# Performance work log

Measured on AMD Instinct MI355X. Metric: run time of the kernel, lower is better.

The kernel has to match this reference:

```python
import jax, jax.numpy as jnp
import numpy as np
from functools import partial

B, T, F, H = 32768, 48, 16, 32  # batch, horizon, feature dim, rnn_size


def setup_inputs() -> dict:
    key = jax.random.key(0)
    ks = jax.random.split(key, 9)
    return {
        "decoder_feature": jax.random.normal(ks[0], (B, T, F), dtype=jnp.float32),
        "decoder_init_input": jax.random.normal(ks[1], (B, 1), dtype=jnp.float32),
        "init_state": jax.random.normal(ks[2], (B, H), dtype=jnp.float32),
        # GRUCell (Keras default reset_after=True): kernel [in_dim, 3H], recurrent [H, 3H], two biases
        "kernel": jax.random.normal(ks[3], (1 + F, 3 * H), dtype=jnp.float32) * 0.1,
        "recurrent_kernel": jax.random.normal(ks[4], (H, 3 * H), dtype=jnp.float32) * 0.1,
        "bias_x": jax.random.normal(ks[5], (3 * H,), dtype=jnp.float32) * 0.1,
        "bias_h": jax.random.normal(ks[6], (3 * H,), dtype=jnp.float32) * 0.1,
        "dense_w": jax.random.normal(ks[7], (H, 1), dtype=jnp.float32) * 0.1,
        "dense_b": jax.random.normal(ks[8], (1,), dtype=jnp.float32) * 0.1,
    }


def reference(decoder_feature, decoder_init_input, init_state,
              kernel, recurrent_kernel, bias_x, bias_h, dense_w, dense_b):
    units = init_state.shape[-1]

    def step(carry, feat_t):
        h, prev_out = carry                              # h: [B,H], prev_out: [B,1]
        x = jnp.concatenate([prev_out, feat_t], axis=1)  # [B, 1+F]
        mx = x @ kernel + bias_x                         # [B, 3H]
        mh = h @ recurrent_kernel + bias_h               # [B, 3H] (reset_after=True)
        xz, xr, xh = jnp.split(mx, 3, axis=1)
        hz, hr, hh_in = jnp.split(mh, 3, axis=1)
        z = jax.nn.sigmoid(xz + hz)
        r = jax.nn.sigmoid(xr + hr)
        hh = jnp.tanh(xh + r * hh_in)
        h_new = z * h + (1.0 - z) * hh                   # GRU output == new state
        out = h_new @ dense_w + dense_b                  # Dense(1): [B,1]
        return (h_new, out), out

    feats = jnp.transpose(decoder_feature, (1, 0, 2))    # [T,B,F] time-major for scan
    _, outs = jax.lax.scan(step, (init_state, decoder_init_input), feats)
    return jnp.transpose(outs, (1, 0, 2))                # [B,T,1]
```

## Files before the change

kernel.cpp:

```cpp
#include <hip/hip_runtime.h>


typedef __attribute__((ext_vector_type(8))) short short8;
typedef __attribute__((ext_vector_type(4))) float f32x4;

constexpr int T_STEPS  = 48;
constexpr int F_DIM    = 16;
constexpr int H_DIM    = 32;
constexpr int ROW_SH   = 40;
constexpr int HX_SH    = 16 * ROW_SH;
constexpr int O_STRIDE = 17;

union S8 { short8 s; unsigned u[4]; };

__device__ __forceinline__ unsigned pk_bf16(float hi, float lo) {
    return __builtin_amdgcn_perm(__float_as_uint(hi) + 0x8000u,
                                 __float_as_uint(lo) + 0x8000u, 0x07060302u);
}
__device__ __forceinline__ short bf16s(float x) {
    return (short)((__float_as_uint(x) + 0x8000u) >> 16);
}
__device__ __forceinline__ float rcpf(float x) { return __builtin_amdgcn_rcpf(x); }
__device__ __forceinline__ float ex2(float x)  { return __builtin_amdgcn_exp2f(x); }
#define MFMA(a, b, c) __builtin_amdgcn_mfma_f32_16x16x32_bf16(a, b, c, 0, 0, 0)
#define SWZ16(v) __int_as_float(__builtin_amdgcn_ds_swizzle(__float_as_int(v), 0x401F))
#define BPERM(a, v) __builtin_amdgcn_ds_bpermute((a), (v))

__global__ __launch_bounds__(128, 4)
void gru_mfma8(const float* __restrict__ feat,
               const float* __restrict__ init_in,
               const float* __restrict__ init_h,
               const float* __restrict__ Wk,
               const float* __restrict__ Rk,
               const float* __restrict__ bx,
               const float* __restrict__ bh,
               const float* __restrict__ dw,
               const float* __restrict__ db,
               float* __restrict__ out)
{
    __shared__ __align__(16) short hx[2 * HX_SH];
    __shared__ float posum[2][2][16];
    __shared__ __align__(16) float obuf[T_STEPS * O_STRIDE];

    const int lane = threadIdx.x & 63;
    const int w    = threadIdx.x >> 6;
    const int ln   = lane & 15;
    const int quad = lane >> 4;
    const int b0   = blockIdx.x * 16;
    const int bpa  = (lane ^ 32) << 2;

    const float SZ = -1.44269504088896340736f;
    const float SC =  2.88539008177792681472f;

    S8 Wfz, Wfr, Wfh, Rfz, Rfr, Rfh;
#pragma unroll
    for (int j = 0; j < 8; ++j) {
        const int k = quad * 8 + j;
        const int n = w * 16 + ln;
        const float wz = (k < 16) ? SZ * Wk[(size_t)(k + 1) * 96 + n]      : 0.0f;
        const float wr = (k < 16) ? SZ * Wk[(size_t)(k + 1) * 96 + 32 + n] : 0.0f;
        const float wh = (k < 16) ? SC * Wk[(size_t)(k + 1) * 96 + 64 + n] : 0.0f;
        Wfz.s[j] = bf16s(wz); Wfr.s[j] = bf16s(wr); Wfh.s[j] = bf16s(wh);
        Rfz.s[j] = bf16s(SZ * Rk[(size_t)k * 96 + n]);
        Rfr.s[j] = bf16s(SZ * Rk[(size_t)k * 96 + 32 + n]);
        Rfh.s[j] = bf16s(SC * Rk[(size_t)k * 96 + 64 + n]);
    }

    float bz4[4], br4[4], bxh4[4], bhh4[4], wz4[4], wr4[4], wh4[4], dw4[4];
#pragma unroll
    for (int i = 0; i < 4; ++i) {
        const int c = w * 16 + quad * 4 + i;
        bz4[i]  = SZ * (bx[c] + bh[c]);
        br4[i]  = SZ * (bx[32 + c] + bh[32 + c]);
        bxh4[i] = SC * bx[64 + c];
        bhh4[i] = SC * bh[64 + c];
        wz4[i]  = SZ * Wk[c];
        wr4[i]  = SZ * Wk[32 + c];
        wh4[i]  = SC * Wk[64 + c];
        dw4[i]  = dw[c];
    }
    const float dbs = db[0];

    float hc[4];
#pragma unroll
    for (int i = 0; i < 4; ++i)
        hc[i] = init_h[(size_t)(b0 + ln) * H_DIM + w * 16 + quad * 4 + i];
    S8 hB;
    {
        const float* hp = init_h + (size_t)(b0 + ln) * H_DIM + quad * 8;
        const f32x4 a = *(const f32x4*)hp;
        const f32x4 b = *(const f32x4*)(hp + 4);
        hB.u[0] = pk_bf16(a[1], a[0]); hB.u[1] = pk_bf16(a[3], a[2]);
        hB.u[2] = pk_bf16(b[1], b[0]); hB.u[3] = pk_bf16(b[3], b[2]);
    }
    float po = init_in[b0 + ln];

    const float* fqb = feat + (size_t)(b0 + ln) * (T_STEPS * F_DIM) + (quad & 1) * 8;
    f32x4 pa0 = *(const f32x4*)(fqb);
    f32x4 pb0 = *(const f32x4*)(fqb + 4);
    f32x4 pa1 = *(const f32x4*)(fqb + F_DIM);
    f32x4 pb1 = *(const f32x4*)(fqb + F_DIM + 4);

    unsigned* hwr = (unsigned*)(hx + ln * ROW_SH + w * 16 + quad * 4);
    const short8* hrd = (const short8*)(hx + ln * ROW_SH + quad * 8);

#define GRU_STEP(T_, P_, PA_, PB_) do {                                        \
        S8 xa;                                                                 \
        xa.u[0] = pk_bf16(PA_[1], PA_[0]); xa.u[1] = pk_bf16(PA_[3], PA_[2]);  \
        xa.u[2] = pk_bf16(PB_[1], PB_[0]); xa.u[3] = pk_bf16(PB_[3], PB_[2]);  \
        const unsigned zm = (quad < 2) ? 0xFFFFFFFFu : 0u;                     \
        xa.u[0] &= zm; xa.u[1] &= zm; xa.u[2] &= zm; xa.u[3] &= zm;            \
            \
        const int t2 = ((T_) + 2 < T_STEPS) ? (T_) + 2 : T_STEPS - 1;          \
        PA_ = *(const f32x4*)(fqb + t2 * F_DIM);                               \
        PB_ = *(const f32x4*)(fqb + t2 * F_DIM + 4);                           \
                                      \
        f32x4 aZ  = {bz4[0],  bz4[1],  bz4[2],  bz4[3]};                       \
        f32x4 aR  = {br4[0],  br4[1],  br4[2],  br4[3]};                       \
        f32x4 aXH = {bxh4[0], bxh4[1], bxh4[2], bxh4[3]};                      \
        f32x4 aHH = {bhh4[0], bhh4[1], bhh4[2], bhh4[3]};                      \
        aZ  = MFMA(Wfz.s, xa.s, aZ);                                           \
        aR  = MFMA(Wfr.s, xa.s, aR);                                           \
        aXH = MFMA(Wfh.s, xa.s, aXH);                                          \
        aZ  = MFMA(Rfz.s, hB.s, aZ);                                           \
        aR  = MFMA(Rfr.s, hB.s, aR);                                           \
        aHH = MFMA(Rfh.s, hB.s, aHH);                                          \
                          \
        float hn[4];                                                           \
        _Pragma("unroll")                                                      \
        for (int i = 0; i < 4; ++i) {                                          \
            const float zz = rcpf(1.0f + ex2(fmaf(po, wz4[i], aZ[i])));        \
            const float rr = rcpf(1.0f + ex2(fmaf(po, wr4[i], aR[i])));        \
            const float vv = fmaf(rr, aHH[i], fmaf(po, wh4[i], aXH[i]));       \
            const float cc = fmaf(-2.0f, rcpf(1.0f + ex2(vv)), 1.0f);          \
            const float h2 = cc + zz * (hc[i] - cc);                           \
            hc[i] = h2;                                                        \
            hn[i] = h2;                                                        \
        }                                                                      \
                          \
        const float d01 = fmaf(hn[0], dw4[0], hn[1] * dw4[1]);                 \
        const float d23 = fmaf(hn[2], dw4[2], hn[3] * dw4[3]);                 \
        float s = d01 + d23;                                                   \
        s += SWZ16(s);                                                         \
        s += __int_as_float(BPERM(bpa, __float_as_int(s)));                    \
                       \
        unsigned* hw = hwr + (P_) * (HX_SH / 2);                               \
        hw[0] = pk_bf16(hn[1], hn[0]);                                         \
        hw[1] = pk_bf16(hn[3], hn[2]);                                         \
        if (lane < 16) posum[P_][w][lane] = s;                                 \
            \
        __builtin_amdgcn_s_waitcnt(0xC07F);                                    \
        __builtin_amdgcn_s_barrier();                                          \
                                      \
        hB.s = hrd[(P_) * (HX_SH / 8)];                                        \
        const float os = posum[P_][1 - w][ln];                                 \
        po = s + os + dbs;                                                     \
        if (w == 0 && lane < 16) obuf[(T_) * O_STRIDE + lane] = po;            \
    } while (0)

    for (int t = 0; t < T_STEPS; t += 2) {
        GRU_STEP(t,     0, pa0, pb0);
        GRU_STEP(t + 1, 1, pa1, pb1);
    }
#undef GRU_STEP

    if (w == 0) {
        const int row = lane >> 2;
        const int tb  = (lane & 3) * 12;
        float* orow = out + (size_t)(b0 + row) * T_STEPS + tb;
#pragma unroll
        for (int k = 0; k < 3; ++k) {
            f32x4 v;
#pragma unroll
            for (int e = 0; e < 4; ++e) v[e] = obuf[(tb + k * 4 + e) * O_STRIDE + row];
            *(f32x4*)(orow + k * 4) = v;
        }
    }
}

extern "C" void kernel_launch(void* const* d_in, const int* in_sizes, int n_in,
                              void* d_out, int out_size, void* d_ws, size_t ws_size,
                              hipStream_t stream) {
    const float* feat    = (const float*)d_in[0];
    const float* init_in = (const float*)d_in[1];
    const float* init_h  = (const float*)d_in[2];
    const float* Wk      = (const float*)d_in[3];
    const float* Rk      = (const float*)d_in[4];
    const float* bx      = (const float*)d_in[5];
    const float* bh      = (const float*)d_in[6];
    const float* dw      = (const float*)d_in[7];
    const float* db      = (const float*)d_in[8];
    float* out           = (float*)d_out;

    const int B = in_sizes[2] / H_DIM;
    dim3 grid((unsigned)(B / 16));
    dim3 block(128);
    hipLaunchKernelGGL(gru_mfma8, grid, block, 0, stream,
                       feat, init_in, init_h, Wk, Rk, bx, bh, dw, db, out);
}
```

Measured before the change: 192.3 us.

## Split GRU step across four waves with LDS gate exchange and two barriers

Each block now runs 256 threads: two waves do the input-projection MFMAs and two do the recurrent-projection MFMAs. Their gate pre-activations go to swizzled LDS planes, and all threads then do an elementwise update of two hidden units each, using a fused single-reciprocal form of the GRU update. This spreads the transcendental work over more lanes and shortens the per-step serial MFMA chain. In exchange it adds a second barrier per step plus extra LDS traffic, which may lengthen the serial recurrence latency.

```diff
diff --git a/kernel.cpp b/kernel.cpp
--- a/kernel.cpp
+++ b/kernel.cpp
@@ -3,13 +3,14 @@
 
 typedef __attribute__((ext_vector_type(8))) short short8;
 typedef __attribute__((ext_vector_type(4))) float f32x4;
-
-constexpr int T_STEPS  = 48;
-constexpr int F_DIM    = 16;
-constexpr int H_DIM    = 32;
-constexpr int ROW_SH   = 40;
-constexpr int HX_SH    = 16 * ROW_SH;
-constexpr int O_STRIDE = 17;
+typedef __attribute__((ext_vector_type(2))) float f32x2;
+
+constexpr int T_STEPS   = 48;
+constexpr int F_DIM     = 16;
+constexpr int H_DIM     = 32;
+constexpr int O_STRIDE  = 17;
+constexpr int HP_STRIDE = 20;
+constexpr int PLANE_DW  = 512;
 
 union S8 { short8 s; unsigned u[4]; };
 
@@ -23,11 +24,10 @@
 __device__ __forceinline__ float rcpf(float x) { return __builtin_amdgcn_rcpf(x); }
 __device__ __forceinline__ float ex2(float x)  { return __builtin_amdgcn_exp2f(x); }
 #define MFMA(a, b, c) __builtin_amdgcn_mfma_f32_16x16x32_bf16(a, b, c, 0, 0, 0)
-#define SWZ16(v) __int_as_float(__builtin_amdgcn_ds_swizzle(__float_as_int(v), 0x401F))
-#define BPERM(a, v) __builtin_amdgcn_ds_bpermute((a), (v))
-
-__global__ __launch_bounds__(128, 4)
-void gru_mfma8(const float* __restrict__ feat,
+#define SWZ(v, off) __int_as_float(__builtin_amdgcn_ds_swizzle(__float_as_int(v), (off)))
+
+__global__ __launch_bounds__(256, 8)
+void gru_mfma9(const float* __restrict__ feat,
                const float* __restrict__ init_in,
                const float* __restrict__ init_h,
                const float* __restrict__ Wk,
@@ -38,135 +38,145 @@
                const float* __restrict__ db,
                float* __restrict__ out)
 {
-    __shared__ __align__(16) short hx[2 * HX_SH];
-    __shared__ float posum[2][2][16];
-    __shared__ __align__(16) float obuf[T_STEPS * O_STRIDE];
-
-    const int lane = threadIdx.x & 63;
-    const int w    = threadIdx.x >> 6;
+    __shared__ __align__(16) float    gp[6 * PLANE_DW];
+    __shared__ __align__(16) unsigned hpl[16 * HP_STRIDE];
+    __shared__ float posum[16];
+    __shared__ __align__(16) float    obuf[T_STEPS * O_STRIDE];
+
+    const int tid  = threadIdx.x;
+    const int lane = tid & 63;
+    const int wv   = tid >> 6;
+    const int half = wv & 1;
+    const int kh   = wv >> 1;
     const int ln   = lane & 15;
     const int quad = lane >> 4;
     const int b0   = blockIdx.x * 16;
-    const int bpa  = (lane ^ 32) << 2;
+    const int ab   = tid >> 4;
+    const int ah   = (tid & 15) * 2;
 
     const float SZ = -1.44269504088896340736f;
     const float SC =  2.88539008177792681472f;
 
-    S8 Wfz, Wfr, Wfh, Rfz, Rfr, Rfh;
+    S8 Az, Ar, Ah;
 #pragma unroll
     for (int j = 0; j < 8; ++j) {
         const int k = quad * 8 + j;
-        const int n = w * 16 + ln;
-        const float wz = (k < 16) ? SZ * Wk[(size_t)(k + 1) * 96 + n]      : 0.0f;
-        const float wr = (k < 16) ? SZ * Wk[(size_t)(k + 1) * 96 + 32 + n] : 0.0f;
-        const float wh = (k < 16) ? SC * Wk[(size_t)(k + 1) * 96 + 64 + n] : 0.0f;
-        Wfz.s[j] = bf16s(wz); Wfr.s[j] = bf16s(wr); Wfh.s[j] = bf16s(wh);
-        Rfz.s[j] = bf16s(SZ * Rk[(size_t)k * 96 + n]);
-        Rfr.s[j] = bf16s(SZ * Rk[(size_t)k * 96 + 32 + n]);
-        Rfh.s[j] = bf16s(SC * Rk[(size_t)k * 96 + 64 + n]);
-    }
-
-    float bz4[4], br4[4], bxh4[4], bhh4[4], wz4[4], wr4[4], wh4[4], dw4[4];
+        const int n = half * 16 + ln;
+        if (kh) {
+            Az.s[j] = bf16s(SZ * Rk[(size_t)k * 96 + n]);
+            Ar.s[j] = bf16s(SZ * Rk[(size_t)k * 96 + 32 + n]);
+            Ah.s[j] = bf16s(SC * Rk[(size_t)k * 96 + 64 + n]);
+        } else {
+            const float wz = (k < 16) ? Wk[(size_t)(k + 1) * 96 + n]      : 0.0f;
+            const float wr = (k < 16) ? Wk[(size_t)(k + 1) * 96 + 32 + n] : 0.0f;
+            const float wh = (k < 16) ? Wk[(size_t)(k + 1) * 96 + 64 + n] : 0.0f;
+            Az.s[j] = bf16s(SZ * wz); Ar.s[j] = bf16s(SZ * wr); Ah.s[j] = bf16s(SC * wh);
+        }
+    }
+
+    f32x4 cz, cr, ch;
 #pragma unroll
     for (int i = 0; i < 4; ++i) {
-        const int c = w * 16 + quad * 4 + i;
-        bz4[i]  = SZ * (bx[c] + bh[c]);
-        br4[i]  = SZ * (bx[32 + c] + bh[32 + c]);
-        bxh4[i] = SC * bx[64 + c];
-        bhh4[i] = SC * bh[64 + c];
-        wz4[i]  = SZ * Wk[c];
-        wr4[i]  = SZ * Wk[32 + c];
-        wh4[i]  = SC * Wk[64 + c];
-        dw4[i]  = dw[c];
-    }
+        const int c = half * 16 + quad * 4 + i;
+        cz[i] = kh ? 0.0f : SZ * (bx[c] + bh[c]);
+        cr[i] = kh ? 0.0f : SZ * (bx[32 + c] + bh[32 + c]);
+        ch[i] = SC * (kh ? bh[64 + c] : bx[64 + c]);
+    }
+
+    float hc0 = init_h[(size_t)(b0 + ab) * H_DIM + ah];
+    float hc1 = init_h[(size_t)(b0 + ab) * H_DIM + ah + 1];
+    const float dw0 = dw[ah], dw1 = dw[ah + 1];
+    const float wzp0 = SZ * Wk[ah],      wzp1 = SZ * Wk[ah + 1];
+    const float wrp0 = SZ * Wk[32 + ah], wrp1 = SZ * Wk[32 + ah + 1];
+    const float whp0 = SC * Wk[64 + ah], whp1 = SC * Wk[64 + ah + 1];
     const float dbs = db[0];
 
-    float hc[4];
-#pragma unroll
-    for (int i = 0; i < 4; ++i)
-        hc[i] = init_h[(size_t)(b0 + ln) * H_DIM + w * 16 + quad * 4 + i];
-    S8 hB;
-    {
-        const float* hp = init_h + (size_t)(b0 + ln) * H_DIM + quad * 8;
-        const f32x4 a = *(const f32x4*)hp;
-        const f32x4 b = *(const f32x4*)(hp + 4);
-        hB.u[0] = pk_bf16(a[1], a[0]); hB.u[1] = pk_bf16(a[3], a[2]);
-        hB.u[2] = pk_bf16(b[1], b[0]); hB.u[3] = pk_bf16(b[3], b[2]);
-    }
-    float po = init_in[b0 + ln];
+    hpl[ab * HP_STRIDE + (ah >> 1)] = pk_bf16(hc1, hc0);
+    if ((tid & 15) == 0) posum[ab] = init_in[b0 + ab];
 
     const float* fqb = feat + (size_t)(b0 + ln) * (T_STEPS * F_DIM) + (quad & 1) * 8;
-    f32x4 pa0 = *(const f32x4*)(fqb);
-    f32x4 pb0 = *(const f32x4*)(fqb + 4);
-    f32x4 pa1 = *(const f32x4*)(fqb + F_DIM);
-    f32x4 pb1 = *(const f32x4*)(fqb + F_DIM + 4);
-
-    unsigned* hwr = (unsigned*)(hx + ln * ROW_SH + w * 16 + quad * 4);
-    const short8* hrd = (const short8*)(hx + ln * ROW_SH + quad * 8);
-
-#define GRU_STEP(T_, P_, PA_, PB_) do {                                        \
-        S8 xa;                                                                 \
-        xa.u[0] = pk_bf16(PA_[1], PA_[0]); xa.u[1] = pk_bf16(PA_[3], PA_[2]);  \
-        xa.u[2] = pk_bf16(PB_[1], PB_[0]); xa.u[3] = pk_bf16(PB_[3], PB_[2]);  \
-        const unsigned zm = (quad < 2) ? 0xFFFFFFFFu : 0u;                     \
-        xa.u[0] &= zm; xa.u[1] &= zm; xa.u[2] &= zm; xa.u[3] &= zm;            \
-            \
-        const int t2 = ((T_) + 2 < T_STEPS) ? (T_) + 2 : T_STEPS - 1;          \
-        PA_ = *(const f32x4*)(fqb + t2 * F_DIM);                               \
-        PB_ = *(const f32x4*)(fqb + t2 * F_DIM + 4);                           \
-                                      \
-        f32x4 aZ  = {bz4[0],  bz4[1],  bz4[2],  bz4[3]};                       \
-        f32x4 aR  = {br4[0],  br4[1],  br4[2],  br4[3]};                       \
-        f32x4 aXH = {bxh4[0], bxh4[1], bxh4[2], bxh4[3]};                      \
-        f32x4 aHH = {bhh4[0], bhh4[1], bhh4[2], bhh4[3]};                      \
-        aZ  = MFMA(Wfz.s, xa.s, aZ);                                           \
-        aR  = MFMA(Wfr.s, xa.s, aR);                                           \
-        aXH = MFMA(Wfh.s, xa.s, aXH);                                          \
-        aZ  = MFMA(Rfz.s, hB.s, aZ);                                           \
-        aR  = MFMA(Rfr.s, hB.s, aR);                                           \
-        aHH = MFMA(Rfh.s, hB.s, aHH);                                          \
-                          \
-        float hn[4];                                                           \
-        _Pragma("unroll")                                                      \
-        for (int i = 0; i < 4; ++i) {                                          \
-            const float zz = rcpf(1.0f + ex2(fmaf(po, wz4[i], aZ[i])));        \
-            const float rr = rcpf(1.0f + ex2(fmaf(po, wr4[i], aR[i])));        \
-            const float vv = fmaf(rr, aHH[i], fmaf(po, wh4[i], aXH[i]));       \
-            const float cc = fmaf(-2.0f, rcpf(1.0f + ex2(vv)), 1.0f);          \
-            const float h2 = cc + zz * (hc[i] - cc);                           \
-            hc[i] = h2;                                                        \
-            hn[i] = h2;                                                        \
-        }                                                                      \
-                          \
-        const float d01 = fmaf(hn[0], dw4[0], hn[1] * dw4[1]);                 \
-        const float d23 = fmaf(hn[2], dw4[2], hn[3] * dw4[3]);                 \
-        float s = d01 + d23;                                                   \
-        s += SWZ16(s);                                                         \
-        s += __int_as_float(BPERM(bpa, __float_as_int(s)));                    \
-                       \
-        unsigned* hw = hwr + (P_) * (HX_SH / 2);                               \
-        hw[0] = pk_bf16(hn[1], hn[0]);                                         \
-        hw[1] = pk_bf16(hn[3], hn[2]);                                         \
-        if (lane < 16) posum[P_][w][lane] = s;                                 \
-            \
-        __builtin_amdgcn_s_waitcnt(0xC07F);                                    \
-        __builtin_amdgcn_s_barrier();                                          \
-                                      \
-        hB.s = hrd[(P_) * (HX_SH / 8)];                                        \
-        const float os = posum[P_][1 - w][ln];                                 \
-        po = s + os + dbs;                                                     \
-        if (w == 0 && lane < 16) obuf[(T_) * O_STRIDE + lane] = po;            \
-    } while (0)
-
-    for (int t = 0; t < T_STEPS; t += 2) {
-        GRU_STEP(t,     0, pa0, pb0);
-        GRU_STEP(t + 1, 1, pa1, pb1);
-    }
-#undef GRU_STEP
-
-    if (w == 0) {
-        const int row = lane >> 2;
-        const int tb  = (lane & 3) * 12;
+    f32x4 pa, pb;
+    if (!kh) { pa = *(const f32x4*)fqb; pb = *(const f32x4*)(fqb + 4); }
+
+    const int gw  = kh * 3 * PLANE_DW + ln * 32
+                  + ((half * 16 + quad * 4) ^ ((ln & 7) << 2));
+    const int grd = ab * 32 + (ah ^ ((ab & 7) << 2));
+    const int hrd = ln * HP_STRIDE + quad * 4;
+    const int hwr = ab * HP_STRIDE + (ah >> 1);
+
+    __syncthreads();
+    S8 bop;
+    if (kh) bop.s = *(const short8*)&hpl[hrd];
+
+    for (int t = 0; t < T_STEPS; ++t) {
+        if (!kh) {
+            if (quad < 2) {
+                bop.u[0] = pk_bf16(pa[1], pa[0]); bop.u[1] = pk_bf16(pa[3], pa[2]);
+                bop.u[2] = pk_bf16(pb[1], pb[0]); bop.u[3] = pk_bf16(pb[3], pb[2]);
+            } else {
+                bop.u[0] = 0; bop.u[1] = 0; bop.u[2] = 0; bop.u[3] = 0;
+            }
+            const int t1 = (t < T_STEPS - 1) ? t + 1 : t;
+            pa = *(const f32x4*)(fqb + t1 * F_DIM);
+            pb = *(const f32x4*)(fqb + t1 * F_DIM + 4);
+        }
+        f32x4 aZ = cz, aR = cr, aH = ch;
+        aZ = MFMA(Az.s, bop.s, aZ);
+        aR = MFMA(Ar.s, bop.s, aR);
+        aH = MFMA(Ah.s, bop.s, aH);
+        *(f32x4*)&gp[gw]                = aZ;
+        *(f32x4*)&gp[gw + PLANE_DW]     = aR;
+        *(f32x4*)&gp[gw + 2 * PLANE_DW] = aH;
+        __builtin_amdgcn_s_waitcnt(0xC07F);
+        __builtin_amdgcn_s_barrier();
+
+        const float po1 = posum[ab];
+        const f32x2 xz = *(const f32x2*)&gp[grd];
+        const f32x2 xr = *(const f32x2*)&gp[grd + PLANE_DW];
+        const f32x2 xh = *(const f32x2*)&gp[grd + 2 * PLANE_DW];
+        const f32x2 hz = *(const f32x2*)&gp[grd + 3 * PLANE_DW];
+        const f32x2 hr = *(const f32x2*)&gp[grd + 4 * PLANE_DW];
+        const f32x2 hh = *(const f32x2*)&gp[grd + 5 * PLANE_DW];
+
+        float h0n, h1n;
+        {
+            const float Sr = fmaf(po1, wrp0, xr[0] + hr[0]);
+            const float rr = rcpf(1.0f + ex2(Sr));
+            const float vv = fmaf(rr, hh[0], fmaf(po1, whp0, xh[0]));
+            const float Ez = ex2(fmaf(po1, wzp0, xz[0] + hz[0]));
+            const float Dv = 1.0f + ex2(vv);
+            const float num = fmaf(hc0, Dv, (Dv - 2.0f) * Ez);
+            const float den = fmaf(Dv, Ez, Dv);
+            h0n = num * rcpf(den);
+        }
+        {
+            const float Sr = fmaf(po1, wrp1, xr[1] + hr[1]);
+            const float rr = rcpf(1.0f + ex2(Sr));
+            const float vv = fmaf(rr, hh[1], fmaf(po1, whp1, xh[1]));
+            const float Ez = ex2(fmaf(po1, wzp1, xz[1] + hz[1]));
+            const float Dv = 1.0f + ex2(vv);
+            const float num = fmaf(hc1, Dv, (Dv - 2.0f) * Ez);
+            const float den = fmaf(Dv, Ez, Dv);
+            h1n = num * rcpf(den);
+        }
+        hc0 = h0n; hc1 = h1n;
+        hpl[hwr] = pk_bf16(h1n, h0n);
+
+        float s = fmaf(h0n, dw0, h1n * dw1);
+        s += SWZ(s, 0x041F);
+        s += SWZ(s, 0x081F);
+        s += SWZ(s, 0x101F);
+        s += SWZ(s, 0x201F);
+        const float po = s + dbs;
+        if ((tid & 15) == 0) { posum[ab] = po; obuf[t * O_STRIDE + ab] = po; }
+        __builtin_amdgcn_s_waitcnt(0xC07F);
+        __builtin_amdgcn_s_barrier();
+        if (kh) bop.s = *(const short8*)&hpl[hrd];
+    }
+
+    if (tid < 64) {
+        const int row = tid >> 2;
+        const int tb  = (tid & 3) * 12;
         float* orow = out + (size_t)(b0 + row) * T_STEPS + tb;
 #pragma unroll
         for (int k = 0; k < 3; ++k) {
@@ -194,7 +204,7 @@
 
     const int B = in_sizes[2] / H_DIM;
     dim3 grid((unsigned)(B / 16));
-    dim3 block(128);
-    hipLaunchKernelGGL(gru_mfma8, grid, block, 0, stream,
+    dim3 block(256);
+    hipLaunchKernelGGL(gru_mfma9, grid, block, 0, stream,
                        feat, init_in, init_h, Wk, Rk, bx, bh, dw, db, out);
 }
```

Result: slower. 320.7 us (+66.7%).

## Process two batch tiles per block and fold prev-output into MFMA

Applied to the files above, without the earlier changes.

Each block now handles 32 batch rows as two independent 16-row chains, interleaving their MFMAs and activations so each barrier-bound recurrence step carries twice the work and exposes ILP. The previous-output input is folded into the x-side MFMA through the padded K slots, using a hi/lo bf16 split to keep precision. The GRU update is rewritten to use one fewer reciprocal by combining the sigmoid and tanh denominators. The cost is more registers and LDS per block, with launch bounds lowered to 2 blocks per SIMD and half as many blocks in the grid.

```diff
diff --git a/kernel.cpp b/kernel.cpp
--- a/kernel.cpp
+++ b/kernel.cpp
@@ -26,27 +26,27 @@
 #define SWZ16(v) __int_as_float(__builtin_amdgcn_ds_swizzle(__float_as_int(v), 0x401F))
 #define BPERM(a, v) __builtin_amdgcn_ds_bpermute((a), (v))
 
-__global__ __launch_bounds__(128, 4)
-void gru_mfma8(const float* __restrict__ feat,
-               const float* __restrict__ init_in,
-               const float* __restrict__ init_h,
-               const float* __restrict__ Wk,
-               const float* __restrict__ Rk,
-               const float* __restrict__ bx,
-               const float* __restrict__ bh,
-               const float* __restrict__ dw,
-               const float* __restrict__ db,
-               float* __restrict__ out)
+__global__ __launch_bounds__(128, 2)
+void gru_mfma10(const float* __restrict__ feat,
+                const float* __restrict__ init_in,
+                const float* __restrict__ init_h,
+                const float* __restrict__ Wk,
+                const float* __restrict__ Rk,
+                const float* __restrict__ bx,
+                const float* __restrict__ bh,
+                const float* __restrict__ dw,
+                const float* __restrict__ db,
+                float* __restrict__ out)
 {
-    __shared__ __align__(16) short hx[2 * HX_SH];
-    __shared__ float posum[2][2][16];
-    __shared__ __align__(16) float obuf[T_STEPS * O_STRIDE];
+    __shared__ __align__(16) short hx[4 * HX_SH];
+    __shared__ float posumf[2 * 2 * 2 * 16];
+    __shared__ __align__(16) float obuf[2 * T_STEPS * O_STRIDE];
 
     const int lane = threadIdx.x & 63;
     const int w    = threadIdx.x >> 6;
     const int ln   = lane & 15;
     const int quad = lane >> 4;
-    const int b0   = blockIdx.x * 16;
+    const int b0   = blockIdx.x * 32;
     const int bpa  = (lane ^ 32) << 2;
 
     const float SZ = -1.44269504088896340736f;
@@ -57,16 +57,23 @@
     for (int j = 0; j < 8; ++j) {
         const int k = quad * 8 + j;
         const int n = w * 16 + ln;
-        const float wz = (k < 16) ? SZ * Wk[(size_t)(k + 1) * 96 + n]      : 0.0f;
-        const float wr = (k < 16) ? SZ * Wk[(size_t)(k + 1) * 96 + 32 + n] : 0.0f;
-        const float wh = (k < 16) ? SC * Wk[(size_t)(k + 1) * 96 + 64 + n] : 0.0f;
-        Wfz.s[j] = bf16s(wz); Wfr.s[j] = bf16s(wr); Wfh.s[j] = bf16s(wh);
+        float wz = 0.0f, wr = 0.0f, wh = 0.0f;
+        if (k < 16) {
+            wz = Wk[(size_t)(k + 1) * 96 + n];
+            wr = Wk[(size_t)(k + 1) * 96 + 32 + n];
+            wh = Wk[(size_t)(k + 1) * 96 + 64 + n];
+        } else if (k < 18) {
+            wz = Wk[n];
+            wr = Wk[32 + n];
+            wh = Wk[64 + n];
+        }
+        Wfz.s[j] = bf16s(SZ * wz); Wfr.s[j] = bf16s(SZ * wr); Wfh.s[j] = bf16s(SC * wh);
         Rfz.s[j] = bf16s(SZ * Rk[(size_t)k * 96 + n]);
         Rfr.s[j] = bf16s(SZ * Rk[(size_t)k * 96 + 32 + n]);
         Rfh.s[j] = bf16s(SC * Rk[(size_t)k * 96 + 64 + n]);
     }
 
-    float bz4[4], br4[4], bxh4[4], bhh4[4], wz4[4], wr4[4], wh4[4], dw4[4];
+    float bz4[4], br4[4], bxh4[4], bhh4[4], dw4[4];
 #pragma unroll
     for (int i = 0; i < 4; ++i) {
         const int c = w * 16 + quad * 4 + i;
@@ -74,105 +81,161 @@
         br4[i]  = SZ * (bx[32 + c] + bh[32 + c]);
         bxh4[i] = SC * bx[64 + c];
         bhh4[i] = SC * bh[64 + c];
-        wz4[i]  = SZ * Wk[c];
-        wr4[i]  = SZ * Wk[32 + c];
-        wh4[i]  = SC * Wk[64 + c];
         dw4[i]  = dw[c];
     }
     const float dbs = db[0];
 
-    float hc[4];
-#pragma unroll
-    for (int i = 0; i < 4; ++i)
-        hc[i] = init_h[(size_t)(b0 + ln) * H_DIM + w * 16 + quad * 4 + i];
-    S8 hB;
+    float hc0[4], hc1[4];
+#pragma unroll
+    for (int i = 0; i < 4; ++i) {
+        hc0[i] = init_h[(size_t)(b0 + ln) * H_DIM + w * 16 + quad * 4 + i];
+        hc1[i] = init_h[(size_t)(b0 + 16 + ln) * H_DIM + w * 16 + quad * 4 + i];
+    }
+    S8 hB0, hB1;
     {
-        const float* hp = init_h + (size_t)(b0 + ln) * H_DIM + quad * 8;
-        const f32x4 a = *(const f32x4*)hp;
-        const f32x4 b = *(const f32x4*)(hp + 4);
-        hB.u[0] = pk_bf16(a[1], a[0]); hB.u[1] = pk_bf16(a[3], a[2]);
-        hB.u[2] = pk_bf16(b[1], b[0]); hB.u[3] = pk_bf16(b[3], b[2]);
-    }
-    float po = init_in[b0 + ln];
-
-    const float* fqb = feat + (size_t)(b0 + ln) * (T_STEPS * F_DIM) + (quad & 1) * 8;
-    f32x4 pa0 = *(const f32x4*)(fqb);
-    f32x4 pb0 = *(const f32x4*)(fqb + 4);
-    f32x4 pa1 = *(const f32x4*)(fqb + F_DIM);
-    f32x4 pb1 = *(const f32x4*)(fqb + F_DIM + 4);
+        const float* hp0 = init_h + (size_t)(b0 + ln) * H_DIM + quad * 8;
+        const float* hp1 = init_h + (size_t)(b0 + 16 + ln) * H_DIM + quad * 8;
+        f32x4 a = *(const f32x4*)hp0, b = *(const f32x4*)(hp0 + 4);
+        hB0.u[0] = pk_bf16(a[1], a[0]); hB0.u[1] = pk_bf16(a[3], a[2]);
+        hB0.u[2] = pk_bf16(b[1], b[0]); hB0.u[3] = pk_bf16(b[3], b[2]);
+        a = *(const f32x4*)hp1; b = *(const f32x4*)(hp1 + 4);
+        hB1.u[0] = pk_bf16(a[1], a[0]); hB1.u[1] = pk_bf16(a[3], a[2]);
+        hB1.u[2] = pk_bf16(b[1], b[0]); hB1.u[3] = pk_bf16(b[3], b[2]);
+    }
+    float po0 = init_in[b0 + ln];
+    float po1 = init_in[b0 + 16 + ln];
+
+    const float* fq0 = feat + (size_t)(b0 + ln) * (T_STEPS * F_DIM) + (quad & 1) * 8;
+    const float* fq1 = feat + (size_t)(b0 + 16 + ln) * (T_STEPS * F_DIM) + (quad & 1) * 8;
+    f32x4 p0a0 = *(const f32x4*)(fq0);
+    f32x4 p0b0 = *(const f32x4*)(fq0 + 4);
+    f32x4 p0a1 = *(const f32x4*)(fq0 + F_DIM);
+    f32x4 p0b1 = *(const f32x4*)(fq0 + F_DIM + 4);
+    f32x4 p1a0 = *(const f32x4*)(fq1);
+    f32x4 p1b0 = *(const f32x4*)(fq1 + 4);
+    f32x4 p1a1 = *(const f32x4*)(fq1 + F_DIM);
+    f32x4 p1b1 = *(const f32x4*)(fq1 + F_DIM + 4);
 
     unsigned* hwr = (unsigned*)(hx + ln * ROW_SH + w * 16 + quad * 4);
     const short8* hrd = (const short8*)(hx + ln * ROW_SH + quad * 8);
 
-#define GRU_STEP(T_, P_, PA_, PB_) do {                                        \
-        S8 xa;                                                                 \
-        xa.u[0] = pk_bf16(PA_[1], PA_[0]); xa.u[1] = pk_bf16(PA_[3], PA_[2]);  \
-        xa.u[2] = pk_bf16(PB_[1], PB_[0]); xa.u[3] = pk_bf16(PB_[3], PB_[2]);  \
-        const unsigned zm = (quad < 2) ? 0xFFFFFFFFu : 0u;                     \
-        xa.u[0] &= zm; xa.u[1] &= zm; xa.u[2] &= zm; xa.u[3] &= zm;            \
-            \
-        const int t2 = ((T_) + 2 < T_STEPS) ? (T_) + 2 : T_STEPS - 1;          \
-        PA_ = *(const f32x4*)(fqb + t2 * F_DIM);                               \
-        PB_ = *(const f32x4*)(fqb + t2 * F_DIM + 4);                           \
-                                      \
-        f32x4 aZ  = {bz4[0],  bz4[1],  bz4[2],  bz4[3]};                       \
-        f32x4 aR  = {br4[0],  br4[1],  br4[2],  br4[3]};                       \
-        f32x4 aXH = {bxh4[0], bxh4[1], bxh4[2], bxh4[3]};                      \
-        f32x4 aHH = {bhh4[0], bhh4[1], bhh4[2], bhh4[3]};                      \
-        aZ  = MFMA(Wfz.s, xa.s, aZ);                                           \
-        aR  = MFMA(Wfr.s, xa.s, aR);                                           \
-        aXH = MFMA(Wfh.s, xa.s, aXH);                                          \
-        aZ  = MFMA(Rfz.s, hB.s, aZ);                                           \
-        aR  = MFMA(Rfr.s, hB.s, aR);                                           \
-        aHH = MFMA(Rfh.s, hB.s, aHH);                                          \
-                          \
-        float hn[4];                                                           \
+#define STEP2(T_, P_, PA_, PB_, QA_, QB_) do {                                 \
+        S8 xa0, xa1;                                                           \
+        {                                                                      \
+            const unsigned zm = (quad < 2) ? 0xFFFFFFFFu : 0u;                 \
+            xa0.u[0] = pk_bf16(PA_[1], PA_[0]) & zm;                           \
+            xa0.u[1] = pk_bf16(PA_[3], PA_[2]) & zm;                           \
+            xa0.u[2] = pk_bf16(PB_[1], PB_[0]) & zm;                           \
+            xa0.u[3] = pk_bf16(PB_[3], PB_[2]) & zm;                           \
+            xa1.u[0] = pk_bf16(QA_[1], QA_[0]) & zm;                           \
+            xa1.u[1] = pk_bf16(QA_[3], QA_[2]) & zm;                           \
+            xa1.u[2] = pk_bf16(QB_[1], QB_[0]) & zm;                           \
+            xa1.u[3] = pk_bf16(QB_[3], QB_[2]) & zm;                           \
+            if (quad == 2) {            \
+                const float h0 = __uint_as_float(                              \
+                    (__float_as_uint(po0) + 0x8000u) & 0xFFFF0000u);           \
+                const float h1 = __uint_as_float(                              \
+                    (__float_as_uint(po1) + 0x8000u) & 0xFFFF0000u);           \
+                xa0.u[0] = pk_bf16(po0 - h0, h0);                              \
+                xa1.u[0] = pk_bf16(po1 - h1, h1);                              \
+            }                                                                  \
+        }                                                                      \
+        {         \
+            const int t2 = ((T_) + 2 < T_STEPS) ? (T_) + 2 : T_STEPS - 1;      \
+            PA_ = *(const f32x4*)(fq0 + t2 * F_DIM);                           \
+            PB_ = *(const f32x4*)(fq0 + t2 * F_DIM + 4);                       \
+            QA_ = *(const f32x4*)(fq1 + t2 * F_DIM);                           \
+            QB_ = *(const f32x4*)(fq1 + t2 * F_DIM + 4);                       \
+        }                                                                      \
+                                \
+        f32x4 aZ0 = {bz4[0], bz4[1], bz4[2], bz4[3]};                          \
+        f32x4 aR0 = {br4[0], br4[1], br4[2], br4[3]};                          \
+        f32x4 aH0 = {bxh4[0], bxh4[1], bxh4[2], bxh4[3]};                      \
+        f32x4 aG0 = {bhh4[0], bhh4[1], bhh4[2], bhh4[3]};                      \
+        f32x4 aZ1 = aZ0, aR1 = aR0, aH1 = aH0, aG1 = aG0;                      \
+        aZ0 = MFMA(Wfz.s, xa0.s, aZ0);  aZ1 = MFMA(Wfz.s, xa1.s, aZ1);         \
+        aR0 = MFMA(Wfr.s, xa0.s, aR0);  aR1 = MFMA(Wfr.s, xa1.s, aR1);         \
+        aH0 = MFMA(Wfh.s, xa0.s, aH0);  aH1 = MFMA(Wfh.s, xa1.s, aH1);         \
+        aZ0 = MFMA(Rfz.s, hB0.s, aZ0);  aZ1 = MFMA(Rfz.s, hB1.s, aZ1);         \
+        aR0 = MFMA(Rfr.s, hB0.s, aR0);  aR1 = MFMA(Rfr.s, hB1.s, aR1);         \
+        aG0 = MFMA(Rfh.s, hB0.s, aG0);  aG1 = MFMA(Rfh.s, hB1.s, aG1);         \
+                              \
+        float hn0[4], hn1[4];                                                  \
         _Pragma("unroll")                                                      \
         for (int i = 0; i < 4; ++i) {                                          \
-            const float zz = rcpf(1.0f + ex2(fmaf(po, wz4[i], aZ[i])));        \
-            const float rr = rcpf(1.0f + ex2(fmaf(po, wr4[i], aR[i])));        \
-            const float vv = fmaf(rr, aHH[i], fmaf(po, wh4[i], aXH[i]));       \
-            const float cc = fmaf(-2.0f, rcpf(1.0f + ex2(vv)), 1.0f);          \
-            const float h2 = cc + zz * (hc[i] - cc);                           \
-            hc[i] = h2;                                                        \
-            hn[i] = h2;                                                        \
-        }                                                                      \
-                          \
-        const float d01 = fmaf(hn[0], dw4[0], hn[1] * dw4[1]);                 \
-        const float d23 = fmaf(hn[2], dw4[2], hn[3] * dw4[3]);                 \
-        float s = d01 + d23;                                                   \
-        s += SWZ16(s);                                                         \
-        s += __int_as_float(BPERM(bpa, __float_as_int(s)));                    \
-                       \
-        unsigned* hw = hwr + (P_) * (HX_SH / 2);                               \
-        hw[0] = pk_bf16(hn[1], hn[0]);                                         \
-        hw[1] = pk_bf16(hn[3], hn[2]);                                         \
-        if (lane < 16) posum[P_][w][lane] = s;                                 \
-            \
+            {                                                                  \
+                const float Ez = ex2(aZ0[i]);                                  \
+                const float rr = rcpf(1.0f + ex2(aR0[i]));                     \
+                const float vv = fmaf(rr, aG0[i], aH0[i]);                     \
+                const float Dv = 1.0f + ex2(vv);                               \
+                const float num = fmaf(hc0[i], Dv, (Dv - 2.0f) * Ez);          \
+                const float den = fmaf(Dv, Ez, Dv);                            \
+                const float h2 = num * rcpf(den);                              \
+                hc0[i] = h2; hn0[i] = h2;                                      \
+            }                                                                  \
+            {                                                                  \
+                const float Ez = ex2(aZ1[i]);                                  \
+                const float rr = rcpf(1.0f + ex2(aR1[i]));                     \
+                const float vv = fmaf(rr, aG1[i], aH1[i]);                     \
+                const float Dv = 1.0f + ex2(vv);                               \
+                const float num = fmaf(hc1[i], Dv, (Dv - 2.0f) * Ez);          \
+                const float den = fmaf(Dv, Ez, Dv);                            \
+                const float h2 = num * rcpf(den);                              \
+                hc1[i] = h2; hn1[i] = h2;                                      \
+            }                                                                  \
+        }                                                                      \
+                                             \
+        float s0 = fmaf(hn0[0], dw4[0], hn0[1] * dw4[1])                       \
+                 + fmaf(hn0[2], dw4[2], hn0[3] * dw4[3]);                      \
+        float s1 = fmaf(hn1[0], dw4[0], hn1[1] * dw4[1])                       \
+                 + fmaf(hn1[2], dw4[2], hn1[3] * dw4[3]);                      \
+        s0 += SWZ16(s0); s1 += SWZ16(s1);                                      \
+        s0 += __int_as_float(BPERM(bpa, __float_as_int(s0)));                  \
+        s1 += __int_as_float(BPERM(bpa, __float_as_int(s1)));                  \
+                             \
+        {                                                                      \
+            unsigned* hw0 = hwr + (0 * 2 + (P_)) * (HX_SH / 2);                \
+            unsigned* hw1 = hwr + (2 + (P_)) * (HX_SH / 2);                    \
+            hw0[0] = pk_bf16(hn0[1], hn0[0]);                                  \
+            hw0[1] = pk_bf16(hn0[3], hn0[2]);                                  \
+            hw1[0] = pk_bf16(hn1[1], hn1[0]);                                  \
+            hw1[1] = pk_bf16(hn1[3], hn1[2]);                                  \
+            if (lane < 16) {                                                   \
+                posumf[((0 * 2 + (P_)) * 2 + w) * 16 + lane] = s0;             \
+                posumf[((2 + (P_)) * 2 + w) * 16 + lane] = s1;                 \
+            }                                                                  \
+        }                                                                      \
+                \
         __builtin_amdgcn_s_waitcnt(0xC07F);                                    \
         __builtin_amdgcn_s_barrier();                                          \
-                                      \
-        hB.s = hrd[(P_) * (HX_SH / 8)];                                        \
-        const float os = posum[P_][1 - w][ln];                                 \
-        po = s + os + dbs;                                                     \
-        if (w == 0 && lane < 16) obuf[(T_) * O_STRIDE + lane] = po;            \
+                                    \
+        hB0.s = hrd[(0 * 2 + (P_)) * (HX_SH / 8)];                             \
+        hB1.s = hrd[(2 + (P_)) * (HX_SH / 8)];                                 \
+        po0 = s0 + posumf[((0 * 2 + (P_)) * 2 + (1 - w)) * 16 + ln] + dbs;     \
+        po1 = s1 + posumf[((2 + (P_)) * 2 + (1 - w)) * 16 + ln] + dbs;         \
+        if (lane < 16) {                                                       \
+            if (w == 0) obuf[(T_) * O_STRIDE + lane] = po0;                    \
+            else        obuf[T_STEPS * O_STRIDE + (T_) * O_STRIDE + lane] = po1;\
+        }                                                                      \
     } while (0)
 
     for (int t = 0; t < T_STEPS; t += 2) {
-        GRU_STEP(t,     0, pa0, pb0);
-        GRU_STEP(t + 1, 1, pa1, pb1);
-    }
-#undef GRU_STEP
-
-    if (w == 0) {
+        STEP2(t,     0, p0a0, p0b0, p1a0, p1b0);
+        STEP2(t + 1, 1, p0a1, p0b1, p1a1, p1b1);
+    }
+#undef STEP2
+
+    __syncthreads();
+    {
+        const float* ob = obuf + w * (T_STEPS * O_STRIDE);
         const int row = lane >> 2;
         const int tb  = (lane & 3) * 12;
-        float* orow = out + (size_t)(b0 + row) * T_STEPS + tb;
+        float* orow = out + (size_t)(b0 + w * 16 + row) * T_STEPS + tb;
 #pragma unroll
         for (int k = 0; k < 3; ++k) {
             f32x4 v;
 #pragma unroll
-            for (int e = 0; e < 4; ++e) v[e] = obuf[(tb + k * 4 + e) * O_STRIDE + row];
+            for (int e = 0; e < 4; ++e) v[e] = ob[(tb + k * 4 + e) * O_STRIDE + row];
             *(f32x4*)(orow + k * 4) = v;
         }
     }
@@ -193,8 +256,8 @@
     float* out           = (float*)d_out;
 
     const int B = in_sizes[2] / H_DIM;
-    dim3 grid((unsigned)(B / 16));
+    dim3 grid((unsigned)(B / 32));
     dim3 block(128);
-    hipLaunchKernelGGL(gru_mfma8, grid, block, 0, stream,
+    hipLaunchKernelGGL(gru_mfma10, grid, block, 0, stream,
                        feat, init_in, init_h, Wk, Rk, bx, bh, dw, db, out);
 }
```

New measurement: 184.7 us. 1.04x faster.

## Run each 16-row GRU tile in one wavefront with register-resident hidden state

Applied to the files above, without the earlier changes.

Each 16-row batch tile now runs on a single 64-lane wavefront instead of two. A column permutation makes the MFMA output layout match the B-operand layout of the next step, so the hidden state is repacked in registers and the per-step LDS exchange and block barrier go away. The previous-output term is folded into the MFMA as a split-bf16 hi/lo input row, and the z-gate/tanh blend is rewritten to use one reciprocal instead of two. Each wave now issues twice the MFMAs and transcendentals per step, and the single-wave blocks may change occupancy and latency hiding.

```diff
diff --git a/kernel.cpp b/kernel.cpp
--- a/kernel.cpp
+++ b/kernel.cpp
@@ -7,8 +7,6 @@
 constexpr int T_STEPS  = 48;
 constexpr int F_DIM    = 16;
 constexpr int H_DIM    = 32;
-constexpr int ROW_SH   = 40;
-constexpr int HX_SH    = 16 * ROW_SH;
 constexpr int O_STRIDE = 17;
 
 union S8 { short8 s; unsigned u[4]; };
@@ -26,24 +24,21 @@
 #define SWZ16(v) __int_as_float(__builtin_amdgcn_ds_swizzle(__float_as_int(v), 0x401F))
 #define BPERM(a, v) __builtin_amdgcn_ds_bpermute((a), (v))
 
-__global__ __launch_bounds__(128, 4)
-void gru_mfma8(const float* __restrict__ feat,
-               const float* __restrict__ init_in,
-               const float* __restrict__ init_h,
-               const float* __restrict__ Wk,
-               const float* __restrict__ Rk,
-               const float* __restrict__ bx,
-               const float* __restrict__ bh,
-               const float* __restrict__ dw,
-               const float* __restrict__ db,
-               float* __restrict__ out)
+__global__ __launch_bounds__(64, 2)
+void gru_mfma11(const float* __restrict__ feat,
+                const float* __restrict__ init_in,
+                const float* __restrict__ init_h,
+                const float* __restrict__ Wk,
+                const float* __restrict__ Rk,
+                const float* __restrict__ bx,
+                const float* __restrict__ bh,
+                const float* __restrict__ dw,
+                const float* __restrict__ db,
+                float* __restrict__ out)
 {
-    __shared__ __align__(16) short hx[2 * HX_SH];
-    __shared__ float posum[2][2][16];
     __shared__ __align__(16) float obuf[T_STEPS * O_STRIDE];
 
-    const int lane = threadIdx.x & 63;
-    const int w    = threadIdx.x >> 6;
+    const int lane = threadIdx.x;
     const int ln   = lane & 15;
     const int quad = lane >> 4;
     const int b0   = blockIdx.x * 16;
@@ -52,47 +47,55 @@
     const float SZ = -1.44269504088896340736f;
     const float SC =  2.88539008177792681472f;
 
-    S8 Wfz, Wfr, Wfh, Rfz, Rfr, Rfh;
+    const int cA0 = (ln >> 2) * 8 + (ln & 3);
+    const int cA1 = cA0 + 4;
+
+    S8 WzA, WrA, WhA, WzB, WrB, WhB, RzA, RrA, RhA, RzB, RrB, RhB;
 #pragma unroll
     for (int j = 0; j < 8; ++j) {
         const int k = quad * 8 + j;
-        const int n = w * 16 + ln;
-        const float wz = (k < 16) ? SZ * Wk[(size_t)(k + 1) * 96 + n]      : 0.0f;
-        const float wr = (k < 16) ? SZ * Wk[(size_t)(k + 1) * 96 + 32 + n] : 0.0f;
-        const float wh = (k < 16) ? SC * Wk[(size_t)(k + 1) * 96 + 64 + n] : 0.0f;
-        Wfz.s[j] = bf16s(wz); Wfr.s[j] = bf16s(wr); Wfh.s[j] = bf16s(wh);
-        Rfz.s[j] = bf16s(SZ * Rk[(size_t)k * 96 + n]);
-        Rfr.s[j] = bf16s(SZ * Rk[(size_t)k * 96 + 32 + n]);
-        Rfh.s[j] = bf16s(SC * Rk[(size_t)k * 96 + 64 + n]);
-    }
-
-    float bz4[4], br4[4], bxh4[4], bhh4[4], wz4[4], wr4[4], wh4[4], dw4[4];
+        float wzA = 0, wrA = 0, whA = 0, wzB = 0, wrB = 0, whB = 0;
+        if (k < 16) {
+            const float* Wrow = Wk + (size_t)(k + 1) * 96;
+            wzA = Wrow[cA0]; wrA = Wrow[32 + cA0]; whA = Wrow[64 + cA0];
+            wzB = Wrow[cA1]; wrB = Wrow[32 + cA1]; whB = Wrow[64 + cA1];
+        } else if (k < 18) {
+            wzA = Wk[cA0]; wrA = Wk[32 + cA0]; whA = Wk[64 + cA0];
+            wzB = Wk[cA1]; wrB = Wk[32 + cA1]; whB = Wk[64 + cA1];
+        }
+        WzA.s[j] = bf16s(SZ * wzA); WrA.s[j] = bf16s(SZ * wrA); WhA.s[j] = bf16s(SC * whA);
+        WzB.s[j] = bf16s(SZ * wzB); WrB.s[j] = bf16s(SZ * wrB); WhB.s[j] = bf16s(SC * whB);
+        const float* Rrow = Rk + (size_t)k * 96;
+        RzA.s[j] = bf16s(SZ * Rrow[cA0]); RrA.s[j] = bf16s(SZ * Rrow[32 + cA0]);
+        RhA.s[j] = bf16s(SC * Rrow[64 + cA0]);
+        RzB.s[j] = bf16s(SZ * Rrow[cA1]); RrB.s[j] = bf16s(SZ * Rrow[32 + cA1]);
+        RhB.s[j] = bf16s(SC * Rrow[64 + cA1]);
+    }
+
+    f32x4 czA, crA, chA, cgA, czB, crB, chB, cgB, dwA, dwB;
 #pragma unroll
     for (int i = 0; i < 4; ++i) {
-        const int c = w * 16 + quad * 4 + i;
-        bz4[i]  = SZ * (bx[c] + bh[c]);
-        br4[i]  = SZ * (bx[32 + c] + bh[32 + c]);
-        bxh4[i] = SC * bx[64 + c];
-        bhh4[i] = SC * bh[64 + c];
-        wz4[i]  = SZ * Wk[c];
-        wr4[i]  = SZ * Wk[32 + c];
-        wh4[i]  = SC * Wk[64 + c];
-        dw4[i]  = dw[c];
+        const int c0 = quad * 8 + i, c1 = c0 + 4;
+        czA[i] = SZ * (bx[c0] + bh[c0]);           czB[i] = SZ * (bx[c1] + bh[c1]);
+        crA[i] = SZ * (bx[32 + c0] + bh[32 + c0]); crB[i] = SZ * (bx[32 + c1] + bh[32 + c1]);
+        chA[i] = SC * bx[64 + c0];                 chB[i] = SC * bx[64 + c1];
+        cgA[i] = SC * bh[64 + c0];                 cgB[i] = SC * bh[64 + c1];
+        dwA[i] = dw[c0];                           dwB[i] = dw[c1];
     }
     const float dbs = db[0];
 
-    float hc[4];
-#pragma unroll
-    for (int i = 0; i < 4; ++i)
-        hc[i] = init_h[(size_t)(b0 + ln) * H_DIM + w * 16 + quad * 4 + i];
+    f32x4 hcA, hcB;
+#pragma unroll
+    for (int i = 0; i < 4; ++i) {
+        hcA[i] = init_h[(size_t)(b0 + ln) * H_DIM + quad * 8 + i];
+        hcB[i] = init_h[(size_t)(b0 + ln) * H_DIM + quad * 8 + 4 + i];
+    }
     S8 hB;
-    {
-        const float* hp = init_h + (size_t)(b0 + ln) * H_DIM + quad * 8;
-        const f32x4 a = *(const f32x4*)hp;
-        const f32x4 b = *(const f32x4*)(hp + 4);
-        hB.u[0] = pk_bf16(a[1], a[0]); hB.u[1] = pk_bf16(a[3], a[2]);
-        hB.u[2] = pk_bf16(b[1], b[0]); hB.u[3] = pk_bf16(b[3], b[2]);
-    }
+    hB.u[0] = pk_bf16(hcA[1], hcA[0]);
+    hB.u[1] = pk_bf16(hcA[3], hcA[2]);
+    hB.u[2] = pk_bf16(hcB[1], hcB[0]);
+    hB.u[3] = pk_bf16(hcB[3], hcB[2]);
+
     float po = init_in[b0 + ln];
 
     const float* fqb = feat + (size_t)(b0 + ln) * (T_STEPS * F_DIM) + (quad & 1) * 8;
@@ -101,70 +104,83 @@
     f32x4 pa1 = *(const f32x4*)(fqb + F_DIM);
     f32x4 pb1 = *(const f32x4*)(fqb + F_DIM + 4);
 
-    unsigned* hwr = (unsigned*)(hx + ln * ROW_SH + w * 16 + quad * 4);
-    const short8* hrd = (const short8*)(hx + ln * ROW_SH + quad * 8);
-
-#define GRU_STEP(T_, P_, PA_, PB_) do {                                        \
+#define GRU_STEP(T_, PA_, PB_) do {                                            \
         S8 xa;                                                                 \
-        xa.u[0] = pk_bf16(PA_[1], PA_[0]); xa.u[1] = pk_bf16(PA_[3], PA_[2]);  \
-        xa.u[2] = pk_bf16(PB_[1], PB_[0]); xa.u[3] = pk_bf16(PB_[3], PB_[2]);  \
-        const unsigned zm = (quad < 2) ? 0xFFFFFFFFu : 0u;                     \
-        xa.u[0] &= zm; xa.u[1] &= zm; xa.u[2] &= zm; xa.u[3] &= zm;            \
-            \
-        const int t2 = ((T_) + 2 < T_STEPS) ? (T_) + 2 : T_STEPS - 1;          \
-        PA_ = *(const f32x4*)(fqb + t2 * F_DIM);                               \
-        PB_ = *(const f32x4*)(fqb + t2 * F_DIM + 4);                           \
-                                      \
-        f32x4 aZ  = {bz4[0],  bz4[1],  bz4[2],  bz4[3]};                       \
-        f32x4 aR  = {br4[0],  br4[1],  br4[2],  br4[3]};                       \
-        f32x4 aXH = {bxh4[0], bxh4[1], bxh4[2], bxh4[3]};                      \
-        f32x4 aHH = {bhh4[0], bhh4[1], bhh4[2], bhh4[3]};                      \
-        aZ  = MFMA(Wfz.s, xa.s, aZ);                                           \
-        aR  = MFMA(Wfr.s, xa.s, aR);                                           \
-        aXH = MFMA(Wfh.s, xa.s, aXH);                                          \
-        aZ  = MFMA(Rfz.s, hB.s, aZ);                                           \
-        aR  = MFMA(Rfr.s, hB.s, aR);                                           \
-        aHH = MFMA(Rfh.s, hB.s, aHH);                                          \
-                          \
-        float hn[4];                                                           \
+        {                                                                      \
+            const unsigned zm = (quad < 2) ? 0xFFFFFFFFu : 0u;                 \
+            xa.u[0] = pk_bf16(PA_[1], PA_[0]) & zm;                            \
+            xa.u[1] = pk_bf16(PA_[3], PA_[2]) & zm;                            \
+            xa.u[2] = pk_bf16(PB_[1], PB_[0]) & zm;                            \
+            xa.u[3] = pk_bf16(PB_[3], PB_[2]) & zm;                            \
+            if (quad == 2) {            \
+                const float ph = __uint_as_float(                              \
+                    (__float_as_uint(po) + 0x8000u) & 0xFFFF0000u);            \
+                xa.u[0] = pk_bf16(po - ph, ph);                                \
+            }                                                                  \
+        }                                                                      \
+        {                                             \
+            const int t2 = ((T_) + 2 < T_STEPS) ? (T_) + 2 : T_STEPS - 1;      \
+            PA_ = *(const f32x4*)(fqb + t2 * F_DIM);                           \
+            PB_ = *(const f32x4*)(fqb + t2 * F_DIM + 4);                       \
+        }                                                                      \
+                                              \
+        f32x4 aZA = czA, aRA = crA, aHA = chA, aGA = cgA;                      \
+        f32x4 aZB = czB, aRB = crB, aHB = chB, aGB = cgB;                      \
+        aZA = MFMA(WzA.s, xa.s, aZA);  aZB = MFMA(WzB.s, xa.s, aZB);           \
+        aRA = MFMA(WrA.s, xa.s, aRA);  aRB = MFMA(WrB.s, xa.s, aRB);           \
+        aHA = MFMA(WhA.s, xa.s, aHA);  aHB = MFMA(WhB.s, xa.s, aHB);           \
+        aZA = MFMA(RzA.s, hB.s, aZA);  aZB = MFMA(RzB.s, hB.s, aZB);           \
+        aRA = MFMA(RrA.s, hB.s, aRA);  aRB = MFMA(RrB.s, hB.s, aRB);           \
+        aGA = MFMA(RhA.s, hB.s, aGA);  aGB = MFMA(RhB.s, hB.s, aGB);           \
+                                   \
         _Pragma("unroll")                                                      \
         for (int i = 0; i < 4; ++i) {                                          \
-            const float zz = rcpf(1.0f + ex2(fmaf(po, wz4[i], aZ[i])));        \
-            const float rr = rcpf(1.0f + ex2(fmaf(po, wr4[i], aR[i])));        \
-            const float vv = fmaf(rr, aHH[i], fmaf(po, wh4[i], aXH[i]));       \
-            const float cc = fmaf(-2.0f, rcpf(1.0f + ex2(vv)), 1.0f);          \
-            const float h2 = cc + zz * (hc[i] - cc);                           \
-            hc[i] = h2;                                                        \
-            hn[i] = h2;                                                        \
+            {                                                                  \
+                const float Ez = ex2(aZA[i]);                                  \
+                const float rr = rcpf(1.0f + ex2(aRA[i]));                     \
+                const float vv = fmaf(rr, aGA[i], aHA[i]);                     \
+                const float Dv = 1.0f + ex2(vv);                               \
+                const float num = fmaf(hcA[i], Dv, (Dv - 2.0f) * Ez);          \
+                const float den = fmaf(Dv, Ez, Dv);                            \
+                hcA[i] = num * rcpf(den);                                      \
+            }                                                                  \
+            {                                                                  \
+                const float Ez = ex2(aZB[i]);                                  \
+                const float rr = rcpf(1.0f + ex2(aRB[i]));                     \
+                const float vv = fmaf(rr, aGB[i], aHB[i]);                     \
+                const float Dv = 1.0f + ex2(vv);                               \
+                const float num = fmaf(hcB[i], Dv, (Dv - 2.0f) * Ez);          \
+                const float den = fmaf(Dv, Ez, Dv);                            \
+                hcB[i] = num * rcpf(den);                                      \
+            }                                                                  \
         }                                                                      \
-                          \
-        const float d01 = fmaf(hn[0], dw4[0], hn[1] * dw4[1]);                 \
-        const float d23 = fmaf(hn[2], dw4[2], hn[3] * dw4[3]);                 \
-        float s = d01 + d23;                                                   \
+                   \
+        hB.u[0] = pk_bf16(hcA[1], hcA[0]);                                     \
+        hB.u[1] = pk_bf16(hcA[3], hcA[2]);                                     \
+        hB.u[2] = pk_bf16(hcB[1], hcB[0]);                                     \
+        hB.u[3] = pk_bf16(hcB[3], hcB[2]);                                     \
+                   \
+        float s = fmaf(hcA[0], dwA[0], hcA[1] * dwA[1]);                       \
+        s = fmaf(hcA[2], dwA[2], s);                                           \
+        s = fmaf(hcA[3], dwA[3], s);                                           \
+        s = fmaf(hcB[0], dwB[0], s);                                           \
+        s = fmaf(hcB[1], dwB[1], s);                                           \
+        s = fmaf(hcB[2], dwB[2], s);                                           \
+        s = fmaf(hcB[3], dwB[3], s);                                           \
         s += SWZ16(s);                                                         \
         s += __int_as_float(BPERM(bpa, __float_as_int(s)));                    \
-                       \
-        unsigned* hw = hwr + (P_) * (HX_SH / 2);                               \
-        hw[0] = pk_bf16(hn[1], hn[0]);                                         \
-        hw[1] = pk_bf16(hn[3], hn[2]);                                         \
-        if (lane < 16) posum[P_][w][lane] = s;                                 \
-            \
-        __builtin_amdgcn_s_waitcnt(0xC07F);                                    \
-        __builtin_amdgcn_s_barrier();                                          \
-                                      \
-        hB.s = hrd[(P_) * (HX_SH / 8)];                                        \
-        const float os = posum[P_][1 - w][ln];                                 \
-        po = s + os + dbs;                                                     \
-        if (w == 0 && lane < 16) obuf[(T_) * O_STRIDE + lane] = po;            \
+        po = s + dbs;                                                          \
+        if (lane < 16) obuf[(T_) * O_STRIDE + lane] = po;                      \
     } while (0)
 
     for (int t = 0; t < T_STEPS; t += 2) {
-        GRU_STEP(t,     0, pa0, pb0);
-        GRU_STEP(t + 1, 1, pa1, pb1);
+        GRU_STEP(t,     pa0, pb0);
+        GRU_STEP(t + 1, pa1, pb1);
     }
 #undef GRU_STEP
 
-    if (w == 0) {
+    __builtin_amdgcn_s_waitcnt(0xC07F);
+    {
         const int row = lane >> 2;
         const int tb  = (lane & 3) * 12;
         float* orow = out + (size_t)(b0 + row) * T_STEPS + tb;
@@ -194,7 +210,7 @@
 
     const int B = in_sizes[2] / H_DIM;
     dim3 grid((unsigned)(B / 16));
-    dim3 block(128);
-    hipLaunchKernelGGL(gru_mfma8, grid, block, 0, stream,
+    dim3 block(64);
+    hipLaunchKernelGGL(gru_mfma11, grid, block, 0, stream,
                        feat, init_in, init_h, Wk, Rk, bx, bh, dw, db, out);
 }
```

Result: faster. 173.1 us (-10.0%).
